# Performance work log

Measured on AMD Instinct MI355X. Metric: run time of the kernel, lower is better.

## Reference

```python
import jax, jax.numpy as jnp
import numpy as np

NUM_CODES = 1024
CODE_DIM = 256
COMMIT_W = 0.25
EPS = 1e-5
ENT_LO, ENT_HI = 0.5, 0.9
ENT_W = 0.1
VAR_FLOOR = 0.05
VAR_W = 1e-3
DECORR_W = 1e-3


def setup_inputs() -> dict:
    key = jax.random.key(0)
    k1, k2, k3 = jax.random.split(key, 3)
    inputs = jax.random.normal(k1, (16, 2048, CODE_DIM), dtype=jnp.float32)
    weight = jax.random.normal(k2, (NUM_CODES, CODE_DIM), dtype=jnp.float32) * 0.1
    usage_counts = jax.random.uniform(k3, (NUM_CODES,), dtype=jnp.float32)
    return {"inputs": inputs, "weight": weight, "usage_counts": usage_counts}


def reference(inputs, weight, usage_counts):
    K, D = weight.shape
    flat = inputs.reshape(-1, D)  # [N, D]
    # squared euclidean distances [N, K]
    dist = (flat ** 2).sum(axis=1, keepdims=True) - 2.0 * flat @ weight.T + (weight ** 2).sum(axis=1)
    idx = jnp.argmin(dist, axis=1)  # [N]
    quant = weight[idx].reshape(inputs.shape)

    commitment_loss = COMMIT_W * jnp.mean((jax.lax.stop_gradient(quant) - inputs) ** 2)
    # straight-through estimator
    quant_ste = inputs + jax.lax.stop_gradient(quant - inputs)

    # usage entropy regularizer
    probs = usage_counts + EPS
    probs = probs / jnp.maximum(probs.sum(), EPS * K)
    usage_entropy = -jnp.sum(probs * jnp.log(probs + EPS)) / np.log(float(K)).astype(np.float32)
    gap = jnp.where(usage_entropy < ENT_LO, ENT_LO - usage_entropy,
                    jnp.where(usage_entropy > ENT_HI, usage_entropy - ENT_HI, 0.0))
    entropy_loss = ENT_W * gap ** 2

    # variance floor penalty on codebook
    variance = jnp.var(weight, axis=0)
    variance_loss = VAR_W * jnp.mean(jax.nn.relu(VAR_FLOOR - variance))

    # decorrelation penalty
    wc = weight - weight.mean(axis=0, keepdims=True)
    cov = wc.T @ wc / float(K)  # [D, D]
    off_diag = cov - jnp.diag(jnp.diag(cov))
    decorrelation_loss = DECORR_W * jnp.mean(off_diag ** 2)

    total_loss = commitment_loss + entropy_loss + variance_loss + decorrelation_loss
    indices = idx.reshape(inputs.shape[:-1])
    return (quant_ste, indices, total_loss, commitment_loss, entropy_loss,
            variance_loss, decorrelation_loss, usage_entropy)
```

## Files before the change

### kernel.cpp

```cpp
#include <hip/hip_runtime.h>
#include <math.h>

#define DIMS   256
#define KCODES 1024
#define NTOT   32768
#define TAU    4.0e-4f

typedef __bf16 bf16x8 __attribute__((ext_vector_type(8)));
typedef float  f32x4  __attribute__((ext_vector_type(4)));

#define WS_COMMIT   0
#define WS_FLAGCNT  1
#define WS_DECORR   2
#define WS_COLSUM   16
#define WS_COLSQ    272
#define WS_WSQ      1024
#define WS_XSQ      2048
#define WS_FLAGS    34816
#define WS_CAND1    67584
#define WS_CAND2    329728
#define WS_CANDI    591872
#define WS_WP       854016

#define OUT_Q    0
#define OUT_IDX  8388608
#define OUT_SCAL 8421376


__global__ __launch_bounds__(256) void prep_kernel(const float* __restrict__ X,
                                                   const float* __restrict__ W,
                                                   __bf16* __restrict__ Xp,
                                                   __bf16* __restrict__ Wp2,
                                                   float* ws) {
  int b = blockIdx.x;
  int tid = threadIdx.x;
  if (b < 1056) {
    __shared__ float sqred[256];
    bool isW = b >= 1024;
    const float* src = isW ? W : X;
    __bf16* dst = isW ? Wp2 : Xp;
    int sqoff = isW ? WS_WSQ : WS_XSQ;
    int bb = isW ? b - 1024 : b;
    int kt = tid >> 5, mtl = (tid >> 4) & 1, lc = tid & 15;
    int row = bb * 32 + mtl * 16 + lc;
    int bt = row >> 7, c = row & 127;
    int wv = c >> 6, t = (c >> 4) & 3;
    size_t hibase = ((((size_t)(bt * 8 + kt) * 2 + wv) * 4 + t) * 2) * 512;
    const float* s = src + (size_t)row * DIMS + kt * 32;
    float sq = 0.f;
    #pragma unroll
    for (int kq = 0; kq < 4; kq++) {
      float4 u = *(const float4*)(s + kq * 8);
      float4 v = *(const float4*)(s + kq * 8 + 4);
      float f[8] = {u.x, u.y, u.z, u.w, v.x, v.y, v.z, v.w};
      bf16x8 hi, lo;
      #pragma unroll
      for (int e = 0; e < 8; e++) {
        __bf16 h = (__bf16)f[e];
        hi[e] = h;
        lo[e] = (__bf16)(f[e] - (float)h);
        sq = fmaf(f[e], f[e], sq);
      }
      size_t off = (size_t)(kq * 16 + lc) * 8;
      *(bf16x8*)&dst[hibase + off] = hi;
      *(bf16x8*)&dst[hibase + 512 + off] = lo;
    }
    sqred[tid] = sq;
    __syncthreads();
    if (tid < 32) {
      float s8 = 0.f;
      #pragma unroll
      for (int k = 0; k < 8; k++) s8 += sqred[k * 32 + tid];
      ws[sqoff + bb * 32 + tid] = s8;
    }
  } else {
    __shared__ float wi_s[KCODES];
    __shared__ float red2[256];
    __shared__ float miB;
    __shared__ float red[4];
    int i0 = b - 1056;
    #pragma unroll
    for (int q = 0; q < 4; q++) {
      int row = q * 256 + tid;
      wi_s[row] = W[(size_t)row * DIMS + i0];
    }
    __syncthreads();
    float pm = 0.f;
    #pragma unroll
    for (int q = 0; q < 4; q++) pm += wi_s[tid * 4 + q];
    red2[tid] = pm;
    __syncthreads();
    if (tid == 0) {
      float s = 0.f;
      for (int k = 0; k < 256; k++) s += red2[k];
      miB = s * (1.0f / 1024.0f);
    }
    int j = tid;
    float a0 = 0.f, sj = 0.f, sqj = 0.f;
    for (int k = 0; k < KCODES; k += 4) {
      #pragma unroll
      for (int u = 0; u < 4; u++) {
        float wj = W[(size_t)(k + u) * DIMS + j];
        a0 = fmaf(wi_s[k + u], wj, a0);
        sj += wj;
        sqj = fmaf(wj, wj, sqj);
      }
    }
    if (j == i0) {
      ws[WS_COLSUM + i0] = sj;
      ws[WS_COLSQ + i0] = sqj;
    }
    __syncthreads();
    const float inv = 1.0f / 1024.0f;
    float mj = sj * inv;
    float v = 0.f;
    float c0 = a0 * inv - miB * mj;
    if (i0 != j) v = c0 * c0;
    #pragma unroll
    for (int m = 32; m >= 1; m >>= 1) v += __shfl_xor(v, m);
    if ((j & 63) == 0) red[j >> 6] = v;
    __syncthreads();
    if (j == 0) atomicAdd(&ws[WS_DECORR], (red[0] + red[1]) + (red[2] + red[3]));
  }
}

__device__ __forceinline__ void stage16(const __bf16* g, __bf16* l) {
  __builtin_amdgcn_global_load_lds(
      (const __attribute__((address_space(1))) void*)g,
      (__attribute__((address_space(3))) void*)l, 16, 0, 0);
}

__global__ __launch_bounds__(512, 4) void pass1_kernel(const __bf16* __restrict__ Xp,
                                                       const __bf16* __restrict__ Wp2,
                                                       float* ws) {
  __shared__ __align__(16) __bf16 buf[16384];
  __shared__ float wsqs[128];
  __shared__ float d1L[256];
  __shared__ float d2L[256];
  __shared__ int   i1L[256];

  int tid = threadIdx.x;
  int lane = tid & 63, wave = tid >> 6;
  int wm = wave >> 1, wn = wave & 1;
  int quad = lane >> 4, col = lane & 15;
  int l = blockIdx.x;
  int x = l & 7;
  int j = l >> 3;
  int bm = x * 32 + (j & 15) + (j >> 7) * 16;
  int bn = (j >> 4) & 7;
  int rowBase = bm * 128, cb = bn * 128;

  if (tid < 128) wsqs[tid] = ws[WS_WSQ + cb + tid];

  f32x4 acc[2][4];
  #pragma unroll
  for (int i = 0; i < 2; i++)
    #pragma unroll
    for (int jj = 0; jj < 4; jj++) acc[i][jj] = (f32x4){0.f, 0.f, 0.f, 0.f};

  const __bf16* aSrc = Xp + (size_t)bm * 65536;
  const __bf16* bSrc = Wp2 + (size_t)bn * 65536;

  const int aFragBase = ((wm >> 1) * 8 + (wm & 1) * 4) * 512;

  #pragma unroll
  for (int kt = 0; kt < 8; kt++) {
    __syncthreads();
    stage16(aSrc + kt * 8192 + tid * 8, buf + tid * 8);
    stage16(aSrc + kt * 8192 + 4096 + tid * 8, buf + 4096 + tid * 8);
    stage16(bSrc + kt * 8192 + tid * 8, buf + 8192 + tid * 8);
    stage16(bSrc + kt * 8192 + 4096 + tid * 8, buf + 12288 + tid * 8);
    __syncthreads();

    const __bf16* bA = buf + aFragBase + lane * 8;
    const __bf16* bB = buf + 8192 + wn * 4096 + lane * 8;
    bf16x8 Bf[4][2];
    #pragma unroll
    for (int nt = 0; nt < 4; nt++) {
      Bf[nt][0] = *(const bf16x8*)(bB + nt * 1024);
      Bf[nt][1] = *(const bf16x8*)(bB + nt * 1024 + 512);
    }
    #pragma unroll
    for (int mt = 0; mt < 2; mt++) {
      bf16x8 A0 = *(const bf16x8*)(bA + mt * 1024);
      bf16x8 A1 = *(const bf16x8*)(bA + mt * 1024 + 512);
      #pragma unroll
      for (int nt = 0; nt < 4; nt++) {
        acc[mt][nt] = __builtin_amdgcn_mfma_f32_16x16x32_bf16(A0, Bf[nt][0], acc[mt][nt], 0, 0, 0);
        acc[mt][nt] = __builtin_amdgcn_mfma_f32_16x16x32_bf16(A0, Bf[nt][1], acc[mt][nt], 0, 0, 0);
        acc[mt][nt] = __builtin_amdgcn_mfma_f32_16x16x32_bf16(A1, Bf[nt][0], acc[mt][nt], 0, 0, 0);
      }
    }
  }
  __syncthreads();

  #pragma unroll
  for (int mt = 0; mt < 2; mt++) {
    #pragma unroll
    for (int r = 0; r < 4; r++) {
      float d1 = 3.0e38f, d2 = 3.0e38f;
      int i1 = 0;
      #pragma unroll
      for (int nt = 0; nt < 4; nt++) {
        int lc = wn * 64 + nt * 16 + col;
        float d = wsqs[lc] - 2.0f * acc[mt][nt][r];
        int g = cb + lc;
        if (d < d1) { d2 = d1; d1 = d; i1 = g; }
        else if (d < d2) d2 = d;
      }
      #pragma unroll
      for (int m = 1; m < 16; m <<= 1) {
        float od1 = __shfl_xor(d1, m);
        int oi1 = __shfl_xor(i1, m);
        float od2 = __shfl_xor(d2, m);
        if (od1 < d1 || (od1 == d1 && oi1 < i1)) {
          d2 = fminf(d1, fminf(d2, od2));
          d1 = od1; i1 = oi1;
        } else {
          d2 = fminf(od1, fminf(d2, od2));
        }
      }
      if (col == 0) {
        int lr = wm * 32 + mt * 16 + quad * 4 + r;
        d1L[lr * 2 + wn] = d1;
        d2L[lr * 2 + wn] = d2;
        i1L[lr * 2 + wn] = i1;
      }
    }
  }
  __syncthreads();
  if (tid < 128) {
    float a1 = d1L[tid * 2], a2 = d2L[tid * 2];
    int ai = i1L[tid * 2];
    float b1 = d1L[tid * 2 + 1], b2 = d2L[tid * 2 + 1];
    int bi = i1L[tid * 2 + 1];
    float m1, m2; int mi;
    if (b1 < a1 || (b1 == a1 && bi < ai)) { m1 = b1; mi = bi; m2 = fminf(a1, b2); }
    else { m1 = a1; mi = ai; m2 = fminf(b1, a2); }
    int o = bn * NTOT + rowBase + tid;
    ws[WS_CAND1 + o] = m1;
    ws[WS_CAND2 + o] = m2;
    ((int*)ws)[WS_CANDI + o] = mi;
  }
}

__global__ __launch_bounds__(256) void pass2_kernel(const float* __restrict__ W,
                                                    float* __restrict__ outQ,
                                                    float* __restrict__ outIdx, float* ws) {
  __shared__ float p1L[4][64];
  __shared__ float p2L[4][64];
  __shared__ int   piL[4][64];
  __shared__ int   idx_s[64];
  int tid = threadIdx.x;
  int r0 = blockIdx.x * 64;
  int grp = tid >> 6, rl = tid & 63;
  int row = r0 + rl;
  const float* c1 = ws + WS_CAND1;
  const float* c2 = ws + WS_CAND2;
  const int* ci = (const int*)ws + WS_CANDI;
  {
    int oa = (2 * grp) * NTOT + row;
    int ob = (2 * grp + 1) * NTOT + row;
    float a1 = c1[oa], a2 = c2[oa];
    int ai = ci[oa];
    float b1 = c1[ob], b2 = c2[ob];
    int bi = ci[ob];
    float m1, m2; int mi;
    if (b1 < a1 || (b1 == a1 && bi < ai)) { m1 = b1; mi = bi; m2 = fminf(a1, b2); }
    else { m1 = a1; mi = ai; m2 = fminf(a2, b1); }
    p1L[grp][rl] = m1;
    p2L[grp][rl] = m2;
    piL[grp][rl] = mi;
  }
  __syncthreads();
  if (tid < 64) {
    float m1 = p1L[0][tid], m2 = p2L[0][tid];
    int mi = piL[0][tid];
    #pragma unroll
    for (int w = 1; w < 4; w++) {
      float b1 = p1L[w][tid], b2 = p2L[w][tid];
      int bi = piL[w][tid];
      if (b1 < m1 || (b1 == m1 && bi < mi)) { m2 = fminf(m1, b2); m1 = b1; mi = bi; }
      else { m2 = fminf(m2, b1); }
    }
    int rw = r0 + tid;
    outIdx[rw] = (float)mi;
    idx_s[tid] = mi;
    int* wsI = (int*)ws;
    if (m2 - m1 < TAU) {
      int p = atomicAdd(&wsI[WS_FLAGCNT], 1);
      wsI[WS_FLAGS + p] = rw;
    }
    float partial = ws[WS_XSQ + rw] + m1;
    #pragma unroll
    for (int m = 32; m >= 1; m >>= 1) partial += __shfl_xor(partial, m);
    if (tid == 0) atomicAdd(&ws[WS_COMMIT], partial);
  }
  __syncthreads();
  int wave = tid >> 6, lane = tid & 63;
  #pragma unroll 4
  for (int i = 0; i < 16; i++) {
    int rr = wave * 16 + i;
    int ix = idx_s[rr];
    float4 v = ((const float4*)(W + (size_t)ix * DIMS))[lane];
    ((float4*)(outQ + (size_t)(r0 + rr) * DIMS))[lane] = v;
  }
}

__global__ __launch_bounds__(256) void refine_kernel(const float* __restrict__ X,
                                                     const float* __restrict__ W,
                                                     float* __restrict__ outQ,
                                                     float* __restrict__ outIdx, float* ws,
                                                     const float* __restrict__ U,
                                                     float* __restrict__ out) {
  __shared__ float xs[DIMS];
  __shared__ double dm[256];
  __shared__ int im[256];
  __shared__ int chosen;
  int tid = threadIdx.x;
  if (blockIdx.x == 512) {
    __shared__ float red[256];
    float s = 0.f;
    for (int e = tid; e < KCODES; e += 256) s += U[e] + 1e-5f;
    red[tid] = s;
    __syncthreads();
    for (int st = 128; st >= 1; st >>= 1) {
      if (tid < st) red[tid] += red[tid + st];
      __syncthreads();
    }
    float S = red[0];
    __syncthreads();
    float denom = fmaxf(S, 1e-5f * 1024.0f);
    float h = 0.f;
    for (int e = tid; e < KCODES; e += 256) {
      float p = (U[e] + 1e-5f) / denom;
      h += p * logf(p + 1e-5f);
    }
    red[tid] = h;
    __syncthreads();
    for (int st = 128; st >= 1; st >>= 1) {
      if (tid < st) red[tid] += red[tid + st];
      __syncthreads();
    }
    float H = -red[0] / 6.93147180559945f;
    __syncthreads();
    float m = ws[WS_COLSUM + tid] * (1.0f / 1024.0f);
    float var = ws[WS_COLSQ + tid] * (1.0f / 1024.0f) - m * m;
    float r = 0.05f - var;
    red[tid] = r > 0.f ? r : 0.f;
    __syncthreads();
    for (int st = 128; st >= 1; st >>= 1) {
      if (tid < st) red[tid] += red[tid + st];
      __syncthreads();
    }
    if (tid == 0) {
      float varloss = 1e-3f * (red[0] / 256.0f);
      float gap = H < 0.5f ? (0.5f - H) : (H > 0.9f ? (H - 0.9f) : 0.0f);
      float entloss = 0.1f * gap * gap;
      float commit = 0.25f * ws[WS_COMMIT] / 8388608.0f;
      float dec = 1e-3f * ws[WS_DECORR] / 65536.0f;
      float* sc = out + OUT_SCAL;
      sc[0] = commit + entloss + varloss + dec;
      sc[1] = commit;
      sc[2] = entloss;
      sc[3] = varloss;
      sc[4] = dec;
      sc[5] = H;
    }
    return;
  }
  const int* wsI = (const int*)ws;
  int cnt = wsI[WS_FLAGCNT];
  const int* list = wsI + WS_FLAGS;
  for (int f = blockIdx.x; f < cnt; f += 512) {
    int row = list[f];
    __syncthreads();
    if (tid < 64) ((float4*)xs)[tid] = ((const float4*)(X + (size_t)row * DIMS))[tid];
    __syncthreads();
    double bd = 1.0e300;
    int bi = 0;
    for (int jj = 0; jj < 4; jj++) {
      int c = tid + 256 * jj;
      double a0 = 0.0, a1 = 0.0, a2 = 0.0, a3 = 0.0;
      const float* wr = W + (size_t)c * DIMS;
      #pragma unroll 4
      for (int d4 = 0; d4 < 64; d4++) {
        float4 w = ((const float4*)wr)[d4];
        float4 x = ((const float4*)xs)[d4];
        double e0 = (double)x.x - (double)w.x;
        double e1 = (double)x.y - (double)w.y;
        double e2 = (double)x.z - (double)w.z;
        double e3 = (double)x.w - (double)w.w;
        a0 += e0 * e0; a1 += e1 * e1; a2 += e2 * e2; a3 += e3 * e3;
      }
      double s = (a0 + a1) + (a2 + a3);
      if (s < bd) { bd = s; bi = c; }
    }
    dm[tid] = bd; im[tid] = bi;
    __syncthreads();
    for (int st = 128; st >= 1; st >>= 1) {
      if (tid < st) {
        if (dm[tid + st] < dm[tid] || (dm[tid + st] == dm[tid] && im[tid + st] < im[tid])) {
          dm[tid] = dm[tid + st]; im[tid] = im[tid + st];
        }
      }
      __syncthreads();
    }
    if (tid == 0) { chosen = im[0]; outIdx[row] = (float)im[0]; }
    __syncthreads();
    int ix = chosen;
    if (tid < 64)
      ((float4*)(outQ + (size_t)row * DIMS))[tid] = ((const float4*)(W + (size_t)ix * DIMS))[tid];
  }
}

extern "C" void kernel_launch(void* const* d_in, const int* in_sizes, int n_in, void* d_out,
                              int out_size, void* d_ws, size_t ws_size, hipStream_t stream) {
  const float* X = (const float*)d_in[0];
  const float* W = (const float*)d_in[1];
  const float* U = (const float*)d_in[2];
  float* out = (float*)d_out;
  float* ws = (float*)d_ws;
  __bf16* Xp = (__bf16*)(out + OUT_Q);
  __bf16* Wp2 = (__bf16*)(ws + WS_WP);

  hipMemsetAsync(d_ws, 0, 12, stream);
  prep_kernel<<<1312, 256, 0, stream>>>(X, W, Xp, Wp2, ws);
  pass1_kernel<<<2048, 512, 0, stream>>>(Xp, Wp2, ws);
  pass2_kernel<<<512, 256, 0, stream>>>(W, out + OUT_Q, out + OUT_IDX, ws);
  refine_kernel<<<513, 256, 0, stream>>>(X, W, out + OUT_Q, out + OUT_IDX, ws, U, out);
}
```

Baseline: 219.8 us.

## Fuse pass2 and refine into one cooperative kernel with a grid sync

Merges the argmin-merge/gather pass and the refine/scalar pass into a single cooperative kernel separated by grid.sync(), which removes one kernel launch boundary. The workspace memset is dropped and prep_kernel now zeroes the counters instead. The decorrelation atomicAdd is replaced by per-column partials that are reduced in the scalar block. The risks are the cost of a cooperative launch and grid sync, a requirement that all 512 blocks be co-resident, and the refine loop losing one block's worth of stride. There is also a possible race: prep block 0 zeroes counters that other blocks don't touch until later kernels, so that part is fine.

```diff
diff --git a/kernel.cpp b/kernel.cpp
--- a/kernel.cpp
+++ b/kernel.cpp
@@ -1,5 +1,8 @@
 #include <hip/hip_runtime.h>
+#include <hip/hip_cooperative_groups.h>
 #include <math.h>
+
+namespace cg = cooperative_groups;
 
 #define DIMS   256
 #define KCODES 1024
@@ -11,9 +14,9 @@
 
 #define WS_COMMIT   0
 #define WS_FLAGCNT  1
-#define WS_DECORR   2
 #define WS_COLSUM   16
 #define WS_COLSQ    272
+#define WS_DECP     528
 #define WS_WSQ      1024
 #define WS_XSQ      2048
 #define WS_FLAGS    34816
@@ -36,6 +39,10 @@
   int tid = threadIdx.x;
   if (b < 1056) {
     __shared__ float sqred[256];
+    if (b == 0 && tid == 0) {
+      ws[WS_COMMIT] = 0.f;
+      ((int*)ws)[WS_FLAGCNT] = 0;
+    }
     bool isW = b >= 1024;
     const float* src = isW ? W : X;
     __bf16* dst = isW ? Wp2 : Xp;
@@ -120,7 +127,7 @@
     for (int m = 32; m >= 1; m >>= 1) v += __shfl_xor(v, m);
     if ((j & 63) == 0) red[j >> 6] = v;
     __syncthreads();
-    if (j == 0) atomicAdd(&ws[WS_DECORR], (red[0] + red[1]) + (red[2] + red[3]));
+    if (j == 0) ws[WS_DECP + i0] = (red[0] + red[1]) + (red[2] + red[3]);
   }
 }
 
@@ -244,82 +251,85 @@
   }
 }
 
-__global__ __launch_bounds__(256) void pass2_kernel(const float* __restrict__ W,
-                                                    float* __restrict__ outQ,
-                                                    float* __restrict__ outIdx, float* ws) {
+__global__ __launch_bounds__(256, 2) void tail_kernel(const float* __restrict__ W,
+                                                      float* __restrict__ outQ,
+                                                      float* __restrict__ outIdx,
+                                                      float* ws,
+                                                      const float* __restrict__ X,
+                                                      const float* __restrict__ U,
+                                                      float* __restrict__ out) {
   __shared__ float p1L[4][64];
   __shared__ float p2L[4][64];
   __shared__ int   piL[4][64];
   __shared__ int   idx_s[64];
-  int tid = threadIdx.x;
-  int r0 = blockIdx.x * 64;
-  int grp = tid >> 6, rl = tid & 63;
-  int row = r0 + rl;
-  const float* c1 = ws + WS_CAND1;
-  const float* c2 = ws + WS_CAND2;
-  const int* ci = (const int*)ws + WS_CANDI;
-  {
-    int oa = (2 * grp) * NTOT + row;
-    int ob = (2 * grp + 1) * NTOT + row;
-    float a1 = c1[oa], a2 = c2[oa];
-    int ai = ci[oa];
-    float b1 = c1[ob], b2 = c2[ob];
-    int bi = ci[ob];
-    float m1, m2; int mi;
-    if (b1 < a1 || (b1 == a1 && bi < ai)) { m1 = b1; mi = bi; m2 = fminf(a1, b2); }
-    else { m1 = a1; mi = ai; m2 = fminf(a2, b1); }
-    p1L[grp][rl] = m1;
-    p2L[grp][rl] = m2;
-    piL[grp][rl] = mi;
-  }
-  __syncthreads();
-  if (tid < 64) {
-    float m1 = p1L[0][tid], m2 = p2L[0][tid];
-    int mi = piL[0][tid];
-    #pragma unroll
-    for (int w = 1; w < 4; w++) {
-      float b1 = p1L[w][tid], b2 = p2L[w][tid];
-      int bi = piL[w][tid];
-      if (b1 < m1 || (b1 == m1 && bi < mi)) { m2 = fminf(m1, b2); m1 = b1; mi = bi; }
-      else { m2 = fminf(m2, b1); }
-    }
-    int rw = r0 + tid;
-    outIdx[rw] = (float)mi;
-    idx_s[tid] = mi;
-    int* wsI = (int*)ws;
-    if (m2 - m1 < TAU) {
-      int p = atomicAdd(&wsI[WS_FLAGCNT], 1);
-      wsI[WS_FLAGS + p] = rw;
-    }
-    float partial = ws[WS_XSQ + rw] + m1;
-    #pragma unroll
-    for (int m = 32; m >= 1; m >>= 1) partial += __shfl_xor(partial, m);
-    if (tid == 0) atomicAdd(&ws[WS_COMMIT], partial);
-  }
-  __syncthreads();
-  int wave = tid >> 6, lane = tid & 63;
-  #pragma unroll 4
-  for (int i = 0; i < 16; i++) {
-    int rr = wave * 16 + i;
-    int ix = idx_s[rr];
-    float4 v = ((const float4*)(W + (size_t)ix * DIMS))[lane];
-    ((float4*)(outQ + (size_t)(r0 + rr) * DIMS))[lane] = v;
-  }
-}
-
-__global__ __launch_bounds__(256) void refine_kernel(const float* __restrict__ X,
-                                                     const float* __restrict__ W,
-                                                     float* __restrict__ outQ,
-                                                     float* __restrict__ outIdx, float* ws,
-                                                     const float* __restrict__ U,
-                                                     float* __restrict__ out) {
   __shared__ float xs[DIMS];
   __shared__ double dm[256];
   __shared__ int im[256];
   __shared__ int chosen;
+  __shared__ float red[256];
+
+  cg::grid_group grid = cg::this_grid();
   int tid = threadIdx.x;
-  if (blockIdx.x == 512) {
-    __shared__ float red[256];
+
+  {
+    int r0 = blockIdx.x * 64;
+    int grp = tid >> 6, rl = tid & 63;
+    int row = r0 + rl;
+    const float* c1 = ws + WS_CAND1;
+    const float* c2 = ws + WS_CAND2;
+    const int* ci = (const int*)ws + WS_CANDI;
+    {
+      int oa = (2 * grp) * NTOT + row;
+      int ob = (2 * grp + 1) * NTOT + row;
+      float a1 = c1[oa], a2 = c2[oa];
+      int ai = ci[oa];
+      float b1 = c1[ob], b2 = c2[ob];
+      int bi = ci[ob];
+      float m1, m2; int mi;
+      if (b1 < a1 || (b1 == a1 && bi < ai)) { m1 = b1; mi = bi; m2 = fminf(a1, b2); }
+      else { m1 = a1; mi = ai; m2 = fminf(a2, b1); }
+      p1L[grp][rl] = m1;
+      p2L[grp][rl] = m2;
+      piL[grp][rl] = mi;
+    }
+    __syncthreads();
+    if (tid < 64) {
+      float m1 = p1L[0][tid], m2 = p2L[0][tid];
+      int mi = piL[0][tid];
+      #pragma unroll
+      for (int w = 1; w < 4; w++) {
+        float b1 = p1L[w][tid], b2 = p2L[w][tid];
+        int bi = piL[w][tid];
+        if (b1 < m1 || (b1 == m1 && bi < mi)) { m2 = fminf(m1, b2); m1 = b1; mi = bi; }
+        else { m2 = fminf(m2, b1); }
+      }
+      int rw = r0 + tid;
+      outIdx[rw] = (float)mi;
+      idx_s[tid] = mi;
+      int* wsI = (int*)ws;
+      if (m2 - m1 < TAU) {
+        int p = atomicAdd(&wsI[WS_FLAGCNT], 1);
+        wsI[WS_FLAGS + p] = rw;
+      }
+      float partial = ws[WS_XSQ + rw] + m1;
+      #pragma unroll
+      for (int m = 32; m >= 1; m >>= 1) partial += __shfl_xor(partial, m);
+      if (tid == 0) atomicAdd(&ws[WS_COMMIT], partial);
+    }
+    __syncthreads();
+    int wave = tid >> 6, lane = tid & 63;
+    #pragma unroll 4
+    for (int i = 0; i < 16; i++) {
+      int rr = wave * 16 + i;
+      int ix = idx_s[rr];
+      float4 v = ((const float4*)(W + (size_t)ix * DIMS))[lane];
+      ((float4*)(outQ + (size_t)(r0 + rr) * DIMS))[lane] = v;
+    }
+  }
+
+  grid.sync();
+
+  if (blockIdx.x == 511) {
     float s = 0.f;
     for (int e = tid; e < KCODES; e += 256) s += U[e] + 1e-5f;
     red[tid] = s;
@@ -353,12 +363,20 @@
       if (tid < st) red[tid] += red[tid + st];
       __syncthreads();
     }
+    float varsum = red[0];
+    __syncthreads();
+    red[tid] = ws[WS_DECP + tid];
+    __syncthreads();
+    for (int st = 128; st >= 1; st >>= 1) {
+      if (tid < st) red[tid] += red[tid + st];
+      __syncthreads();
+    }
     if (tid == 0) {
-      float varloss = 1e-3f * (red[0] / 256.0f);
+      float varloss = 1e-3f * (varsum / 256.0f);
       float gap = H < 0.5f ? (0.5f - H) : (H > 0.9f ? (H - 0.9f) : 0.0f);
       float entloss = 0.1f * gap * gap;
       float commit = 0.25f * ws[WS_COMMIT] / 8388608.0f;
-      float dec = 1e-3f * ws[WS_DECORR] / 65536.0f;
+      float dec = 1e-3f * red[0] / 65536.0f;
       float* sc = out + OUT_SCAL;
       sc[0] = commit + entloss + varloss + dec;
       sc[1] = commit;
@@ -372,7 +390,7 @@
   const int* wsI = (const int*)ws;
   int cnt = wsI[WS_FLAGCNT];
   const int* list = wsI + WS_FLAGS;
-  for (int f = blockIdx.x; f < cnt; f += 512) {
+  for (int f = blockIdx.x; f < cnt; f += 511) {
     int row = list[f];
     __syncthreads();
     if (tid < 64) ((float4*)xs)[tid] = ((const float4*)(X + (size_t)row * DIMS))[tid];
@@ -424,9 +442,12 @@
   __bf16* Xp = (__bf16*)(out + OUT_Q);
   __bf16* Wp2 = (__bf16*)(ws + WS_WP);
 
-  hipMemsetAsync(d_ws, 0, 12, stream);
   prep_kernel<<<1312, 256, 0, stream>>>(X, W, Xp, Wp2, ws);
   pass1_kernel<<<2048, 512, 0, stream>>>(Xp, Wp2, ws);
-  pass2_kernel<<<512, 256, 0, stream>>>(W, out + OUT_Q, out + OUT_IDX, ws);
-  refine_kernel<<<513, 256, 0, stream>>>(X, W, out + OUT_Q, out + OUT_IDX, ws, U, out);
+
+  float* outQ = out + OUT_Q;
+  float* outIdx = out + OUT_IDX;
+  void* args[] = {(void*)&W, (void*)&outQ, (void*)&outIdx, (void*)&ws,
+                  (void*)&X, (void*)&U, (void*)&out};
+  hipLaunchCooperativeKernel((void*)tail_kernel, dim3(512), dim3(256), args, 0, stream);
 }
```

Result: slower. 311.0 us (+41.5%).
